# Performance work log

Hardware: AMD Instinct MI355X
Metric: run time of the kernel (lower is better)

Reference implementation:

```python
import jax, jax.numpy as jnp
import numpy as np

U = 4096        # n_users
I = 16384       # n_items
D = 64          # embed_dim
N = U + I       # interaction-graph nodes
NE_I = 524288   # interaction edges (nonzeros of norm_inter_graph)
NE_S = 65536    # social edges
L_INTER = 3     # LightGCN layers on user-item graph
L_SOC = 2       # WeightGCN layers (graph powers) on social graph
NEG_INF = jnp.float32(-1e30)


def setup_inputs() -> dict:
    key = jax.random.key(0)
    ks = jax.random.split(key, 13)
    return {
        'user_emb': jax.random.normal(ks[0], (U, D), jnp.float32) * 0.1,
        'item_emb': jax.random.normal(ks[1], (I, D), jnp.float32) * 0.1,
        'inter_vals': jax.random.uniform(ks[2], (NE_I,), jnp.float32) * 0.05,  # D^-1/2 A D^-1/2 values
        'Wa': jax.random.normal(ks[3], (D, D), jnp.float32) * 0.1,
        'Wb': jax.random.normal(ks[4], (D, D), jnp.float32) * 0.1,
        'w1': jax.random.normal(ks[5], (2 * D, D), jnp.float32) * 0.1,
        'b1': jnp.zeros((D,), jnp.float32),
        'w2': jax.random.normal(ks[6], (D, 1), jnp.float32) * 0.1,
        'b2': jnp.zeros((1,), jnp.float32),
        'inter_rows': jax.random.randint(ks[7], (NE_I,), 0, N, jnp.int32),
        'inter_cols': jax.random.randint(ks[8], (NE_I,), 0, N, jnp.int32),
        'social_rows': jax.random.randint(ks[9], (NE_S,), 0, U, jnp.int32),
        'social_cols': jax.random.randint(ks[10], (NE_S,), 0, U, jnp.int32),
    }


def _spmm(rows, cols, vals, x, n):
    # sparse [n,n] @ dense [n,d] via gather + segment_sum (torch.sparse.mm)
    return jax.ops.segment_sum(vals[:, None] * x[cols], rows, num_segments=n)


def _lightgcn(rows, cols, vals, embed, n, n_layers):
    embs = [embed]
    h = embed
    for _ in range(n_layers):
        h = _spmm(rows, cols, vals, h, n)
        embs.append(h)
    return jnp.mean(jnp.stack(embs, axis=1), axis=1)  # [n, d]


def _masked_row_softmax(g, m):
    # torch.sparse.softmax: softmax over stored (structural) entries per row
    logits = jnp.where(m, g, NEG_INF)
    s = jax.nn.softmax(logits, axis=1)
    return jnp.where(m.any(axis=1, keepdims=True), s, 0.0)


def reference(user_emb, item_emb, inter_vals, Wa, Wb, w1, b1, w2, b2,
              inter_rows, inter_cols, social_rows, social_cols):
    # ---- LightGCN on user-item interaction graph ----
    inter_emb = jnp.concatenate([user_emb, item_emb], axis=0)           # [N, D]
    inter_out = _lightgcn(inter_rows, inter_cols, inter_vals, inter_emb, N, L_INTER)
    user_e, item_e = inter_out[:U], inter_out[U:]

    # ---- edge-activation MLP (infer_activation): h = cols, t = rows ----
    feat = jnp.concatenate([user_emb[social_cols] @ Wa,
                            user_emb[social_rows] @ Wb], axis=1)        # [NE_S, 2D]
    hid = jax.nn.relu(feat @ w1 + b1)
    p = (hid @ w2 + b2)[:, 0]
    edge_w = jax.nn.sigmoid(p)                                          # [NE_S]

    # ---- weighted social graph (duplicates coalesce by sum) ----
    A = jnp.zeros((U, U), jnp.float32).at[social_rows, social_cols].add(edge_w)
    B = (A > 0).astype(jnp.float32)  # structural pattern (non-diff)

    # ---- WeightGCN: graph powers + per-row sparse softmax ----
    graphs, masks = [A], [A > 0]
    g_prev, b_prev = A, B
    for _ in range(L_SOC - 1):
        g_prev = g_prev @ A
        b_prev = b_prev @ B
        graphs.append(g_prev)
        masks.append(b_prev > 0)
    sembs = [user_e]
    for g, m in zip(graphs, masks):
        sembs.append(_masked_row_softmax(g, m) @ user_e)
    social_e2 = jnp.mean(jnp.stack(sembs, axis=1), axis=1)              # [U, D]

    # ---- final user embedding (bpr_loss path) ----
    return user_e + social_e2
```

## Files before the change

### kernel.cpp

```cpp
#include <hip/hip_runtime.h>
#include <hip/hip_bf16.h>

#define U_    4096
#define I_    16384
#define D_    64
#define N_    20480
#define NEI   524288
#define NES   65536
#define CAPI  96
#define RCAPS 64
#define SEG   384

__global__ __launch_bounds__(256) void init_wab2_kernel(int* __restrict__ cnt, int* __restrict__ skv,
                                                        const float* __restrict__ Wa,
                                                        const float* __restrict__ Wb,
                                                        const float* __restrict__ w1,
                                                        float* __restrict__ Wa2, float* __restrict__ Wb2) {
    int b = blockIdx.x;
    if (b < 1024) {
        int tid = b * 256 + threadIdx.x;
        int stride = 1024 * 256;
        for (int o = tid; o < N_; o += stride) cnt[o] = 0;
        for (int o = tid; o < U_ * RCAPS; o += stride) ((int2*)skv)[o] = make_int2(-1, 0);
    } else {
        int o = (b - 1024) * 256 + threadIdx.x;
        int mat = o >> 12;
        int i = (o >> 6) & 63;
        int j = o & 63;
        const float* M  = mat ? Wb : Wa;
        const float* W1 = w1 + mat * 64 * 64;
        float s = 0.f;
        #pragma unroll 8
        for (int k = 0; k < 64; ++k) s += M[i * 64 + k] * W1[k * 64 + j];
        (mat ? Wb2 : Wa2)[i * 64 + j] = s;
    }
}

__global__ void scatter_i_kernel(const int* __restrict__ rows, const int* __restrict__ cols,
                                 const float* __restrict__ vals,
                                 int* __restrict__ cnt, int2* __restrict__ ed) {
    int e = blockIdx.x * 256 + threadIdx.x;
    int r = rows[e];
    int pos = atomicAdd(&cnt[r], 1);
    if (pos < CAPI) ed[(size_t)r * CAPI + pos] = make_int2(cols[e], __float_as_int(vals[e]));
}

__global__ __launch_bounds__(256) void spmm1_pab_kernel(const int* __restrict__ cnt, const int2* __restrict__ ed,
                                                        const float* __restrict__ ue, const float* __restrict__ ie,
                                                        float* __restrict__ h1,
                                                        const float* __restrict__ Wa2, const float* __restrict__ Wb2,
                                                        float* __restrict__ Pa, float* __restrict__ Pb) {
    int b = blockIdx.x;
    int wv = threadIdx.x >> 6, lane = threadIdx.x & 63;
    if (b < 5120) {
        int w = b * 4 + wv;
        int n = cnt[w]; if (n > CAPI) n = CAPI;
        const int2* row = ed + (size_t)w * CAPI;
        float acc = 0.f;
        #pragma unroll 4
        for (int j = 0; j < n; ++j) {
            int2 e = row[j];
            int c = e.x; float v = __int_as_float(e.y);
            const float* xp = (c < U_) ? (ue + (size_t)c * D_) : (ie + (size_t)(c - U_) * D_);
            acc += v * xp[lane];
        }
        h1[(size_t)w * D_ + lane] = acc;
    } else {
        int w = (b - 5120) * 4 + wv;
        float x = ue[w * 64 + lane];
        float accA = 0.f, accB = 0.f;
        #pragma unroll 8
        for (int k = 0; k < 64; ++k) {
            float xk = __shfl(x, k);
            accA += xk * Wa2[k * 64 + lane];
            accB += xk * Wb2[k * 64 + lane];
        }
        Pa[w * 64 + lane] = accA;
        Pb[w * 64 + lane] = accB;
    }
}

__global__ __launch_bounds__(256) void spmm2_edge_kernel(const int* __restrict__ cnt, const int2* __restrict__ ed,
                                                         const float* __restrict__ x, float* __restrict__ y,
                                                         const int* __restrict__ sr, const int* __restrict__ sc,
                                                         const float* __restrict__ Pa, const float* __restrict__ Pb,
                                                         const float* __restrict__ b1, const float* __restrict__ w2,
                                                         const float* __restrict__ b2,
                                                         int* __restrict__ skv) {
    int b = blockIdx.x;
    if (b < 5120) {
        int wv = threadIdx.x >> 6, lane = threadIdx.x & 63;
        int w = b * 4 + wv;
        int n = cnt[w]; if (n > CAPI) n = CAPI;
        const int2* row = ed + (size_t)w * CAPI;
        float acc = 0.f;
        #pragma unroll 4
        for (int j = 0; j < n; ++j) {
            int2 e = row[j];
            acc += __int_as_float(e.y) * x[(size_t)e.x * D_ + lane];
        }
        y[(size_t)w * D_ + lane] = acc;
    } else {
        int w = (b - 5120) * 16 + (threadIdx.x >> 4);
        int q = threadIdx.x & 15;
        int r = sr[w], c = sc[w];
        float4 pa = ((const float4*)Pa)[c * 16 + q];
        float4 pb = ((const float4*)Pb)[r * 16 + q];
        float4 bb = ((const float4*)b1)[q];
        float4 ww = ((const float4*)w2)[q];
        float hx = fmaxf(pa.x + pb.x + bb.x, 0.f);
        float hy = fmaxf(pa.y + pb.y + bb.y, 0.f);
        float hz = fmaxf(pa.z + pb.z + bb.z, 0.f);
        float hw = fmaxf(pa.w + pb.w + bb.w, 0.f);
        float t = hx * ww.x + hy * ww.y + hz * ww.z + hw * ww.w;
        t += __shfl_xor(t, 8);
        t += __shfl_xor(t, 4);
        t += __shfl_xor(t, 2);
        t += __shfl_xor(t, 1);
        if (q == 0) {
            float p = t + b2[0];
            float ew = 1.f / (1.f + expf(-p));
            size_t base = (size_t)r * RCAPS;
            int hh = c & (RCAPS - 1);
            for (int probe = 0; probe < RCAPS; ++probe) {
                int prev = atomicCAS(&skv[(base + hh) * 2], -1, c);
                if (prev == -1 || prev == c) { atomicAdd((float*)&skv[(base + hh) * 2 + 1], ew); break; }
                hh = (hh + 1) & (RCAPS - 1);
            }
        }
    }
}

__global__ __launch_bounds__(256) void spmm_last_kernel(const int* __restrict__ cnt, const int2* __restrict__ ed,
                                                        const float* __restrict__ ue,
                                                        const float* __restrict__ h1, const float* __restrict__ h2,
                                                        float* __restrict__ user_e) {
    int w = (blockIdx.x * 256 + threadIdx.x) >> 6;
    int lane = threadIdx.x & 63;
    int n = cnt[w]; if (n > CAPI) n = CAPI;
    const int2* row = ed + (size_t)w * CAPI;
    float acc = 0.f;
    #pragma unroll 4
    for (int j = 0; j < n; ++j) {
        int2 e = row[j];
        acc += __int_as_float(e.y) * h2[(size_t)e.x * D_ + lane];
    }
    size_t o = (size_t)w * D_ + lane;
    user_e[o] = 0.25f * (ue[o] + h1[o] + h2[o] + acc);
}


__device__ __forceinline__ float wave_max_(float v) {
    #pragma unroll
    for (int o = 32; o > 0; o >>= 1) v = fmaxf(v, __shfl_xor(v, o));
    return v;
}
__device__ __forceinline__ float wave_sum_(float v) {
    #pragma unroll
    for (int o = 32; o > 0; o >>= 1) v += __shfl_xor(v, o);
    return v;
}

__global__ __launch_bounds__(256) void social_kernel(const int* __restrict__ skv,
                                                     const float* __restrict__ user_e,
                                                     float* __restrict__ out) {
    __shared__ float row2[U_];
    __shared__ int   list2[4][SEG];
    __shared__ int   kcol_s[RCAPS];
    __shared__ float kval_s[RCAPS];
    __shared__ float wredm[4], wreds[4];
    __shared__ float accw[4][64];
    __shared__ int   nnz_s;

    int i = blockIdx.x, t = threadIdx.x;
    int wv = t >> 6, lane = t & 63;

    {
        float4* r4 = (float4*)row2;
        #pragma unroll
        for (int u = 0; u < 4; ++u) r4[t + 256 * u] = make_float4(0.f, 0.f, 0.f, 0.f);
    }

    if (wv == 0) {
        int2 kv = ((const int2*)skv)[(size_t)i * RCAPS + lane];
        unsigned long long mask = __ballot(kv.x >= 0);
        int pos = __popcll(mask & ((1ull << lane) - 1ull));
        if (kv.x >= 0) { kcol_s[pos] = kv.x; kval_s[pos] = __int_as_float(kv.y); }
        if (lane == 0) nnz_s = __popcll(mask);
    }
    __syncthreads();
    int nnz = nnz_s;

    float kv  = (lane < nnz) ? kval_s[lane] : -1e30f;
    float m1  = wave_max_(kv);
    float ex  = (lane < nnz) ? expf(kv - m1) : 0.f;
    float S1  = wave_sum_(ex);
    float inv1 = (nnz > 0) ? 1.f / S1 : 0.f;

    for (int e = wv; e < nnz; e += 4) {
        int k = kcol_s[e];
        float vk = kval_s[e];
        int2 kv2 = ((const int2*)skv)[(size_t)k * RCAPS + lane];
        if (kv2.x >= 0) atomicAdd(&row2[kv2.x], vk * __int_as_float(kv2.y));
    }

    float acc = 0.f;
    for (int e = wv; e < nnz; e += 4) {
        float p = __shfl(ex, e) * inv1;
        acc += p * user_e[(size_t)kcol_s[e] * D_ + lane];
    }
    __syncthreads();

    int len = 0;
    float lm = 0.f;
    for (int ch = 0; ch < 16; ++ch) {
        int cb = (wv << 10) + (ch << 6);
        float pv = row2[cb + lane];
        lm = fmaxf(lm, pv);
        unsigned long long msk = __ballot(pv > 0.f);
        int pos = __popcll(msk & ((1ull << lane) - 1ull));
        if (pv > 0.f && len + pos < SEG) list2[wv][len + pos] = cb + lane;
        len += __popcll(msk);
    }
    if (len > SEG) len = SEG;
    lm = wave_max_(lm);
    if (lane == 0) wredm[wv] = lm;
    __syncthreads();
    float m2 = fmaxf(fmaxf(wredm[0], wredm[1]), fmaxf(wredm[2], wredm[3]));

    float ls = 0.f;
    for (int e = lane; e < len; e += 64) {
        int c = list2[wv][e];
        float ev = expf(row2[c] - m2);
        row2[c] = ev;
        ls += ev;
    }
    ls = wave_sum_(ls);
    if (lane == 0) wreds[wv] = ls;
    __syncthreads();
    float S2 = wreds[0] + wreds[1] + wreds[2] + wreds[3];
    float inv2 = (S2 > 0.f) ? 1.f / S2 : 0.f;

    #pragma unroll 4
    for (int e = 0; e < len; ++e) {
        int c = list2[wv][e];
        float p = row2[c] * inv2;
        acc += p * user_e[(size_t)c * D_ + lane];
    }
    accw[wv][lane] = acc;
    __syncthreads();
    if (t < 64) {
        float s = accw[0][t] + accw[1][t] + accw[2][t] + accw[3][t];
        float ue = user_e[(size_t)i * D_ + t];
        out[i * D_ + t] = (4.f * ue + s) * (1.f / 3.f);
    }
}


extern "C" void kernel_launch(void* const* d_in, const int* in_sizes, int n_in,
                              void* d_out, int out_size, void* d_ws, size_t ws_size,
                              hipStream_t stream) {
    (void)in_sizes; (void)n_in; (void)out_size; (void)ws_size;
    const float* user_emb  = (const float*)d_in[0];
    const float* item_emb  = (const float*)d_in[1];
    const float* inter_vals= (const float*)d_in[2];
    const float* Wa        = (const float*)d_in[3];
    const float* Wb        = (const float*)d_in[4];
    const float* w1        = (const float*)d_in[5];
    const float* b1        = (const float*)d_in[6];
    const float* w2        = (const float*)d_in[7];
    const float* b2        = (const float*)d_in[8];
    const int* inter_rows  = (const int*)d_in[9];
    const int* inter_cols  = (const int*)d_in[10];
    const int* social_rows = (const int*)d_in[11];
    const int* social_cols = (const int*)d_in[12];
    float* out = (float*)d_out;

    char* w = (char*)d_ws;
    auto alloc = [&](size_t bytes) -> void* {
        void* p = (void*)w;
        w += (bytes + 255) & ~(size_t)255;
        return p;
    };
    float* h1     = (float*)alloc((size_t)N_ * D_ * 4);
    float* h2     = (float*)alloc((size_t)N_ * D_ * 4);
    float* user_e = (float*)alloc((size_t)U_ * D_ * 4);
    float* Pa     = (float*)alloc((size_t)U_ * D_ * 4);
    float* Pb     = (float*)alloc((size_t)U_ * D_ * 4);
    float* Wa2    = (float*)alloc(64 * 64 * 4);
    float* Wb2    = (float*)alloc(64 * 64 * 4);
    int*   cnt    = (int*)alloc((size_t)N_ * 4);
    int2*  ed     = (int2*)alloc((size_t)N_ * CAPI * 8);
    int*   skv    = (int*)alloc((size_t)U_ * RCAPS * 8);

    init_wab2_kernel<<<1056, 256, 0, stream>>>(cnt, skv, Wa, Wb, w1, Wa2, Wb2);
    scatter_i_kernel<<<NEI / 256, 256, 0, stream>>>(inter_rows, inter_cols, inter_vals, cnt, ed);
    spmm1_pab_kernel<<<6144, 256, 0, stream>>>(cnt, ed, user_emb, item_emb, h1, Wa2, Wb2, Pa, Pb);
    spmm2_edge_kernel<<<9216, 256, 0, stream>>>(cnt, ed, h1, h2, social_rows, social_cols,
                                                Pa, Pb, b1, w2, b2, skv);
    spmm_last_kernel<<<1024, 256, 0, stream>>>(cnt, ed, user_emb, h1, h2, user_e);
    social_kernel<<<U_, 256, 0, stream>>>(skv, user_e, out);
}
```

Baseline: 217.3 us.

## Drop softmax max-subtraction, fuse exp into compaction, vectorize social gathers with float4

The social kernel no longer subtracts the row max before exponentiating, because edge weights come from a sigmoid so A and A^2 values are small and bounded. This removes a wave max, a block barrier and a separate exp pass, and lets the exp happen inside the compaction loop. The embedding gathers now use float4 loads, with four rows handled per wave at once and combined through cross-lane shuffles. SEG is also reduced to cut shared memory; rows with more than SEG nonzeros per wave segment would be truncated, and skipping the max subtraction depends on the values staying small enough not to overflow.

Result: faster. 207.3 us (-4.6%).

```diff
diff --git a/kernel.cpp b/kernel.cpp
--- a/kernel.cpp
+++ b/kernel.cpp
@@ -9,7 +9,7 @@
 #define NES   65536
 #define CAPI  96
 #define RCAPS 64
-#define SEG   384
+#define SEG   280
 
 __global__ __launch_bounds__(256) void init_wab2_kernel(int* __restrict__ cnt, int* __restrict__ skv,
                                                         const float* __restrict__ Wa,
@@ -150,11 +150,6 @@
 }
 
 
-__device__ __forceinline__ float wave_max_(float v) {
-    #pragma unroll
-    for (int o = 32; o > 0; o >>= 1) v = fmaxf(v, __shfl_xor(v, o));
-    return v;
-}
 __device__ __forceinline__ float wave_sum_(float v) {
     #pragma unroll
     for (int o = 32; o > 0; o >>= 1) v += __shfl_xor(v, o);
@@ -164,16 +159,17 @@
 __global__ __launch_bounds__(256) void social_kernel(const int* __restrict__ skv,
                                                      const float* __restrict__ user_e,
                                                      float* __restrict__ out) {
-    __shared__ float row2[U_];
-    __shared__ int   list2[4][SEG];
-    __shared__ int   kcol_s[RCAPS];
-    __shared__ float kval_s[RCAPS];
-    __shared__ float wredm[4], wreds[4];
-    __shared__ float accw[4][64];
-    __shared__ int   nnz_s;
+    __shared__ float  row2[U_];
+    __shared__ int    list2[4][SEG];
+    __shared__ int    kcol_s[RCAPS];
+    __shared__ float  kval_s[RCAPS];
+    __shared__ float  wreds[4];
+    __shared__ float4 accw[4][16];
+    __shared__ int    nnz_s;
 
     int i = blockIdx.x, t = threadIdx.x;
     int wv = t >> 6, lane = t & 63;
+    int rg = lane >> 4, q = lane & 15;
 
     {
         float4* r4 = (float4*)row2;
@@ -191,9 +187,7 @@
     __syncthreads();
     int nnz = nnz_s;
 
-    float kv  = (lane < nnz) ? kval_s[lane] : -1e30f;
-    float m1  = wave_max_(kv);
-    float ex  = (lane < nnz) ? expf(kv - m1) : 0.f;
+    float ex  = (lane < nnz) ? expf(kval_s[lane]) : 0.f;
     float S1  = wave_sum_(ex);
     float inv1 = (nnz > 0) ? 1.f / S1 : 0.f;
 
@@ -204,37 +198,32 @@
         if (kv2.x >= 0) atomicAdd(&row2[kv2.x], vk * __int_as_float(kv2.y));
     }
 
-    float acc = 0.f;
-    for (int e = wv; e < nnz; e += 4) {
-        float p = __shfl(ex, e) * inv1;
-        acc += p * user_e[(size_t)kcol_s[e] * D_ + lane];
+    float4 a4 = make_float4(0.f, 0.f, 0.f, 0.f);
+    for (int base = wv * 4; base < nnz; base += 16) {
+        int idx = base + rg;
+        if (idx < nnz) {
+            float p = expf(kval_s[idx]) * inv1;
+            int c = kcol_s[idx];
+            float4 v = ((const float4*)user_e)[(size_t)c * 16 + q];
+            a4.x += p * v.x; a4.y += p * v.y; a4.z += p * v.z; a4.w += p * v.w;
+        }
     }
     __syncthreads();
 
     int len = 0;
-    float lm = 0.f;
+    float ls = 0.f;
     for (int ch = 0; ch < 16; ++ch) {
         int cb = (wv << 10) + (ch << 6);
         float pv = row2[cb + lane];
-        lm = fmaxf(lm, pv);
-        unsigned long long msk = __ballot(pv > 0.f);
+        bool hit = pv > 0.f;
+        float ev = expf(pv);
+        if (hit) { row2[cb + lane] = ev; ls += ev; }
+        unsigned long long msk = __ballot(hit);
         int pos = __popcll(msk & ((1ull << lane) - 1ull));
-        if (pv > 0.f && len + pos < SEG) list2[wv][len + pos] = cb + lane;
+        if (hit && len + pos < SEG) list2[wv][len + pos] = cb + lane;
         len += __popcll(msk);
     }
     if (len > SEG) len = SEG;
-    lm = wave_max_(lm);
-    if (lane == 0) wredm[wv] = lm;
-    __syncthreads();
-    float m2 = fmaxf(fmaxf(wredm[0], wredm[1]), fmaxf(wredm[2], wredm[3]));
-
-    float ls = 0.f;
-    for (int e = lane; e < len; e += 64) {
-        int c = list2[wv][e];
-        float ev = expf(row2[c] - m2);
-        row2[c] = ev;
-        ls += ev;
-    }
     ls = wave_sum_(ls);
     if (lane == 0) wreds[wv] = ls;
     __syncthreads();
@@ -242,17 +231,30 @@
     float inv2 = (S2 > 0.f) ? 1.f / S2 : 0.f;
 
     #pragma unroll 4
-    for (int e = 0; e < len; ++e) {
+    for (int e = rg; e < len; e += 4) {
         int c = list2[wv][e];
         float p = row2[c] * inv2;
-        acc += p * user_e[(size_t)c * D_ + lane];
-    }
-    accw[wv][lane] = acc;
+        float4 v = ((const float4*)user_e)[(size_t)c * 16 + q];
+        a4.x += p * v.x; a4.y += p * v.y; a4.z += p * v.z; a4.w += p * v.w;
+    }
+    #pragma unroll
+    for (int o = 16; o < 64; o <<= 1) {
+        a4.x += __shfl_xor(a4.x, o);
+        a4.y += __shfl_xor(a4.y, o);
+        a4.z += __shfl_xor(a4.z, o);
+        a4.w += __shfl_xor(a4.w, o);
+    }
+    if (rg == 0) accw[wv][q] = a4;
     __syncthreads();
-    if (t < 64) {
-        float s = accw[0][t] + accw[1][t] + accw[2][t] + accw[3][t];
-        float ue = user_e[(size_t)i * D_ + t];
-        out[i * D_ + t] = (4.f * ue + s) * (1.f / 3.f);
+    if (t < 16) {
+        float4 s0 = accw[0][t], s1 = accw[1][t], s2 = accw[2][t], s3 = accw[3][t];
+        float4 ue4 = ((const float4*)user_e)[(size_t)i * 16 + t];
+        float4 r;
+        r.x = (4.f * ue4.x + s0.x + s1.x + s2.x + s3.x) * (1.f / 3.f);
+        r.y = (4.f * ue4.y + s0.y + s1.y + s2.y + s3.y) * (1.f / 3.f);
+        r.z = (4.f * ue4.z + s0.z + s1.z + s2.z + s3.z) * (1.f / 3.f);
+        r.w = (4.f * ue4.w + s0.w + s1.w + s2.w + s3.w) * (1.f / 3.f);
+        ((float4*)out)[(size_t)i * 16 + t] = r;
     }
 }
 
```
